# Optimization experiments

Measured on AMD Instinct MI355X. Metric: run time of the kernel, lower is better.

Reference implementation:

```python
import math
import jax, jax.numpy as jnp
from jax import lax
import numpy as np

B, T, DIM = 2, 1024, 512
EXPAND, D_STATE, CONV_K, NUM_SCALES = 2, 16, 4, 3
D_INNER = EXPAND * DIM
DT_RANK = D_INNER // 16


def parallel_scan_log(log_coeffs, log_values):
    # h_t = a_t*h_{t-1} + b_t via Heinsen log-space scan
    a_star = jnp.cumsum(log_coeffs, axis=1)
    return jnp.exp(a_star + lax.cumlogsumexp(log_values - a_star, axis=1))


def selective_scan(x, dt, A, B_ssm, C_ssm, D_p):
    Bb, Tt, di = x.shape
    ds = A.shape[1]
    dt = jax.nn.softplus(dt)
    dA = jnp.exp(dt[..., None] * A[None, None])                    # (B,T,di,ds)
    dBx = dt[..., None] * B_ssm[:, :, None, :] * x[..., None]      # (B,T,di,ds)
    log_dA = jnp.log(jnp.maximum(dA, 1e-38)).reshape(Bb, Tt, di * ds)
    log_dBx = jnp.log(jnp.maximum(dBx, 1e-38)).reshape(Bb, Tt, di * ds)
    h = parallel_scan_log(log_dA, log_dBx).reshape(Bb, Tt, di, ds)
    return jnp.einsum('bts,btds->btd', C_ssm, h) + D_p * x


def ssm_core(x, conv_w, conv_b, xproj_w, dtproj_w, dtproj_b, A_log, D_p):
    di = x.shape[-1]
    # depthwise causal conv1d: left-pad K-1 (== torch pad K-1 both sides + truncate to T)
    xc = lax.conv_general_dilated(x.transpose(0, 2, 1), conv_w, (1,), [(CONV_K - 1, 0)],
                                  dimension_numbers=('NCH', 'OIH', 'NCH'),
                                  feature_group_count=di)
    xc = jax.nn.silu((xc + conv_b[None, :, None]).transpose(0, 2, 1))
    proj = xc @ xproj_w.T
    dt_raw = proj[..., :DT_RANK]
    B_ssm = proj[..., DT_RANK:DT_RANK + D_STATE]
    C_ssm = proj[..., DT_RANK + D_STATE:]
    dt = dt_raw @ dtproj_w.T + dtproj_b
    A = -jnp.exp(A_log)
    return selective_scan(xc, dt, A, B_ssm, C_ssm, D_p)


def downsample(x, stride):
    if stride == 1:
        return x
    Bb, Tt, Dd = x.shape
    Tt2 = Tt // stride * stride
    return x[:, :Tt2].reshape(Bb, Tt2 // stride, stride, Dd).mean(axis=2)


def upsample(x, T_target):
    Bb, T_src, Dd = x.shape
    if T_src == T_target:
        return x
    factor = math.ceil(T_target / T_src)
    x_up = jnp.repeat(x, factor, axis=1)[:, :T_target]
    if x_up.shape[1] < T_target:
        pad = jnp.broadcast_to(x_up[:, -1:], (Bb, T_target - x_up.shape[1], Dd))
        x_up = jnp.concatenate([x_up, pad], axis=1)
    return x_up


def forward(x, in_proj_w, conv_w, conv_b, xproj_w, dtproj_w, dtproj_b, A_log, D_p,
            scale_weights, cg_w1, cg_w2, out_proj_w, ln_gamma, ln_beta):
    Tt = x.shape[1]
    residual = x
    xz = x @ in_proj_w.T
    x_in, gate = xz[..., :D_INNER], xz[..., D_INNER:]
    outs = []
    for s in range(NUM_SCALES):
        x_s = downsample(x_in, 2 ** s)
        y_s = ssm_core(x_s, conv_w[s], conv_b[s], xproj_w[s], dtproj_w[s],
                       dtproj_b[s], A_log[s], D_p[s])
        outs.append(upsample(y_s, Tt))
    w = jax.nn.softmax(scale_weights)
    fused = sum(w[s] * outs[s] for s in range(NUM_SCALES))
    ctx = jnp.mean(jnp.stack(outs, axis=0), axis=0)
    cg = jax.nn.sigmoid(jax.nn.silu(ctx @ cg_w1.T) @ cg_w2.T)
    fused = fused * cg
    out = (fused * jax.nn.silu(gate)) @ out_proj_w.T
    y = out + residual
    mu = jnp.mean(y, axis=-1, keepdims=True)
    var = jnp.var(y, axis=-1, keepdims=True)
    return (y - mu) / jnp.sqrt(var + 1e-5) * ln_gamma + ln_beta


def setup_inputs():
    key = jax.random.key(0)
    ks = jax.random.split(key, 12)
    x = jax.random.normal(ks[0], (B, T, DIM), jnp.float32)
    in_proj_w = jax.random.normal(ks[1], (2 * D_INNER, DIM), jnp.float32) * (1.0 / math.sqrt(DIM))
    conv_w = jax.random.normal(ks[2], (NUM_SCALES, D_INNER, 1, CONV_K), jnp.float32) * 0.3
    conv_b = jax.random.normal(ks[3], (NUM_SCALES, D_INNER), jnp.float32) * 0.05
    xproj_w = jax.random.normal(ks[4], (NUM_SCALES, DT_RANK + 2 * D_STATE, D_INNER), jnp.float32) * 0.02
    dtproj_w = jax.random.normal(ks[5], (NUM_SCALES, D_INNER, DT_RANK), jnp.float32) * 0.05
    dtproj_b = jax.random.uniform(ks[6], (NUM_SCALES, D_INNER), jnp.float32,
                                  math.log(0.001), math.log(0.1))
    A_log = jnp.broadcast_to(jnp.log(jnp.arange(1, D_STATE + 1, dtype=jnp.float32)),
                             (NUM_SCALES, D_INNER, D_STATE))
    D_p = jnp.ones((NUM_SCALES, D_INNER), jnp.float32)
    scale_weights = jnp.ones((NUM_SCALES,), jnp.float32)
    cg_w1 = jax.random.normal(ks[7], (D_INNER // 2, D_INNER), jnp.float32) * (1.0 / math.sqrt(D_INNER))
    cg_w2 = jax.random.normal(ks[8], (D_INNER, D_INNER // 2), jnp.float32) * (1.0 / math.sqrt(D_INNER // 2))
    out_proj_w = jax.random.normal(ks[9], (DIM, D_INNER), jnp.float32) * (1.0 / math.sqrt(D_INNER))
    ln_gamma = jnp.ones((DIM,), jnp.float32)
    ln_beta = jnp.zeros((DIM,), jnp.float32)
    return {"x": x, "in_proj_w": in_proj_w, "conv_w": conv_w, "conv_b": conv_b,
            "xproj_w": xproj_w, "dtproj_w": dtproj_w, "dtproj_b": dtproj_b,
            "A_log": A_log, "D_p": D_p, "scale_weights": scale_weights,
            "cg_w1": cg_w1, "cg_w2": cg_w2, "out_proj_w": out_proj_w,
            "ln_gamma": ln_gamma, "ln_beta": ln_beta}


def reference(x, in_proj_w, conv_w, conv_b, xproj_w, dtproj_w, dtproj_b, A_log, D_p,
              scale_weights, cg_w1, cg_w2, out_proj_w, ln_gamma, ln_beta):
    return forward(x, in_proj_w, conv_w, conv_b, xproj_w, dtproj_w, dtproj_b, A_log,
                   D_p, scale_weights, cg_w1, cg_w2, out_proj_w, ln_gamma, ln_beta)
```

## Files before the change

### kernel.cpp

```cpp
#include <hip/hip_runtime.h>
#include <hip/hip_bf16.h>

#define BATCH   2
#define SEQ     1024
#define DIMSZ   512
#define DINNER  1024
#define DTRANK  64
#define DSTATE  16
#define CHUNK   32

typedef __hip_bfloat16 bf16;
typedef __attribute__((ext_vector_type(8))) short s8v;
typedef __attribute__((ext_vector_type(4))) float f4v;

constexpr size_t OXI   = 0;
constexpr size_t OIPI  = 2097152;
constexpr size_t OXWI  = 4194304;
constexpr size_t ODTI  = 4784128;
constexpr size_t OC1I  = 5177344;
constexpr size_t OC2I  = 6225920;
constexpr size_t OOPI  = 7274496;
constexpr size_t OPJI  = 8323072;
constexpr size_t OH1I  = 8781824;
constexpr size_t OFGI  = 10878976;

__device__ __forceinline__ float sigmoidf_(float x) { return 1.f / (1.f + __expf(-x)); }
__device__ __forceinline__ float siluf_(float x) { return x * sigmoidf_(x); }
__device__ __forceinline__ void split2(float v, bf16& hi, bf16& lo) {
    hi = __float2bfloat16(v);
    lo = __float2bfloat16(v - __bfloat162float(hi));
}
__device__ __forceinline__ void split_store4i(const float4 v, bf16* __restrict__ p) {
    union { bf16 b[8]; uint4 q; } U;
    split2(v.x, U.b[0], U.b[4]); split2(v.y, U.b[1], U.b[5]);
    split2(v.z, U.b[2], U.b[6]); split2(v.w, U.b[3], U.b[7]);
    *reinterpret_cast<uint4*>(p) = U.q;
}
__device__ __forceinline__ void split_store4(const float4 v,
                                             bf16* __restrict__ ph,
                                             bf16* __restrict__ pl) {
    union { bf16 b[4]; uint2 u; } H, L;
    split2(v.x, H.b[0], L.b[0]); split2(v.y, H.b[1], L.b[1]);
    split2(v.z, H.b[2], L.b[2]); split2(v.w, H.b[3], L.b[3]);
    *reinterpret_cast<uint2*>(ph) = H.u;
    *reinterpret_cast<uint2*>(pl) = L.u;
}

__global__ void split_inputs_kernel(
    const float* __restrict__ x,   const float* __restrict__ ipw,
    const float* __restrict__ xw,  const float* __restrict__ dtw,
    const float* __restrict__ c1,  const float* __restrict__ c2,
    const float* __restrict__ opw, bf16* __restrict__ bws)
{
    int blk = blockIdx.x;
    const float* src; size_t off;
    if (blk < 1024)      { src = x;   off = OXI;  }
    else if (blk < 2048) { src = ipw; off = OIPI; blk -= 1024; }
    else if (blk < 2336) { src = xw;  off = OXWI; blk -= 2048; }
    else if (blk < 2528) { src = dtw; off = ODTI; blk -= 2336; }
    else if (blk < 3040) { src = c1;  off = OC1I; blk -= 2528; }
    else if (blk < 3552) { src = c2;  off = OC2I; blk -= 3040; }
    else                 { src = opw; off = OOPI; blk -= 3552; }
    int i = blk * 1024 + threadIdx.x * 4;
    float4 v = *reinterpret_cast<const float4*>(src + i);
    split_store4i(v, bws + off + (size_t)i * 2);
}

template <int ACT, bool ADD_RES, bool DT_MODE, bool CTX_A, bool GATE3, bool OUT_SPLIT>
__global__ __launch_bounds__(256) void mgemm_kernel(
    const bf16* __restrict__ Ai, int lda, int K,
    const bf16* __restrict__ Bi,
    const float* __restrict__ bias,
    const float* __restrict__ res,
    const float* __restrict__ gxz,
    const float* __restrict__ yy0,
    const float* __restrict__ yy1,
    const float* __restrict__ yy2,
    const float* __restrict__ swp,
    float* __restrict__ C, bf16* __restrict__ Ci, int N)
{
    __shared__ bf16 Ah[64][72], Al[64][72], Bh[64][72], Bl[64][72];

    const int m0 = blockIdx.x * 64;
    const int n0 = blockIdx.y * 64;
    const int tid = threadIdx.x;
    const int wave = tid >> 6;
    const int lane = tid & 63;
    const int wm = (wave >> 1) * 32;
    const int wn = (wave & 1) * 32;
    const int m16 = lane & 15;
    const int q   = lane >> 4;

    int scale = 0;
    if (DT_MODE) scale = (m0 < 2048) ? 0 : ((m0 < 3072) ? 1 : 2);
    const bf16* Bip = DT_MODE ? (Bi + (size_t)scale * 1024 * K * 2) : Bi;
    const float* bias_p = (ACT == 3) ? (DT_MODE ? bias + (size_t)scale * N : bias) : nullptr;

    f4v acc[2][2];
#pragma unroll
    for (int i = 0; i < 2; i++)
#pragma unroll
        for (int j = 0; j < 2; j++)
#pragma unroll
            for (int r = 0; r < 4; r++) acc[i][j][r] = 0.f;

    const int cch = tid & 15;
    const int c4  = cch * 4;
    const int r0  = tid >> 4;

    const float* a0p[4]; const float* a1p[4]; const float* a2p[4];
    const bf16*  aip[4];
#pragma unroll
    for (int p = 0; p < 4; p++) {
        int m = m0 + r0 + p * 16;
        if (CTX_A) {
            int b = m >> 10, t = m & 1023;
            a0p[p] = yy0 + (size_t)m * 1024 + c4;
            a1p[p] = yy1 + (size_t)((b << 9) + (t >> 1)) * 1024 + c4;
            a2p[p] = yy2 + (size_t)((b << 8) + (t >> 2)) * 1024 + c4;
        } else {
            aip[p] = Ai + ((size_t)m * lda + c4) * 2;
        }
    }
    const bf16* Bi_b = Bip + ((size_t)(n0 + r0) * K + c4) * 2;

    const int nkt = K >> 6;
    float4 raf[4]; uint2 rah[4], ral[4], rbh[4], rbl[4];
#pragma unroll
    for (int p = 0; p < 4; p++) {
        if (CTX_A) {
            float4 u = *reinterpret_cast<const float4*>(a0p[p]);
            float4 v = *reinterpret_cast<const float4*>(a1p[p]);
            float4 w = *reinterpret_cast<const float4*>(a2p[p]);
            raf[p] = make_float4((u.x + v.x + w.x) * (1.f / 3.f), (u.y + v.y + w.y) * (1.f / 3.f),
                                 (u.z + v.z + w.z) * (1.f / 3.f), (u.w + v.w + w.w) * (1.f / 3.f));
        } else {
            uint4 ua = *reinterpret_cast<const uint4*>(aip[p]);
            rah[p] = make_uint2(ua.x, ua.y); ral[p] = make_uint2(ua.z, ua.w);
        }
        uint4 ub = *reinterpret_cast<const uint4*>(Bi_b + (size_t)(p * 16) * K * 2);
        rbh[p] = make_uint2(ub.x, ub.y); rbl[p] = make_uint2(ub.z, ub.w);
    }

    for (int kt = 0; kt < nkt; kt++) {
        if (kt) __syncthreads();
#pragma unroll
        for (int p = 0; p < 4; p++) {
            int r = r0 + p * 16;
            if (CTX_A) {
                split_store4(raf[p], &Ah[r][c4], &Al[r][c4]);
            } else {
                *reinterpret_cast<uint2*>(&Ah[r][c4]) = rah[p];
                *reinterpret_cast<uint2*>(&Al[r][c4]) = ral[p];
            }
            *reinterpret_cast<uint2*>(&Bh[r][c4]) = rbh[p];
            *reinterpret_cast<uint2*>(&Bl[r][c4]) = rbl[p];
        }
        __syncthreads();
        if (kt + 1 < nkt) {
            int off = (kt + 1) * 64;
#pragma unroll
            for (int p = 0; p < 4; p++) {
                if (CTX_A) {
                    float4 u = *reinterpret_cast<const float4*>(a0p[p] + off);
                    float4 v = *reinterpret_cast<const float4*>(a1p[p] + off);
                    float4 w = *reinterpret_cast<const float4*>(a2p[p] + off);
                    raf[p] = make_float4((u.x + v.x + w.x) * (1.f / 3.f), (u.y + v.y + w.y) * (1.f / 3.f),
                                         (u.z + v.z + w.z) * (1.f / 3.f), (u.w + v.w + w.w) * (1.f / 3.f));
                } else {
                    uint4 ua = *reinterpret_cast<const uint4*>(aip[p] + (size_t)off * 2);
                    rah[p] = make_uint2(ua.x, ua.y); ral[p] = make_uint2(ua.z, ua.w);
                }
                uint4 ub = *reinterpret_cast<const uint4*>(Bi_b + ((size_t)(p * 16) * K + off) * 2);
                rbh[p] = make_uint2(ub.x, ub.y); rbl[p] = make_uint2(ub.z, ub.w);
            }
        }
#pragma unroll
        for (int kk = 0; kk < 2; kk++) {
            const int col = kk * 32 + q * 8;
            s8v ah[2], al[2], bh[2], bl[2];
#pragma unroll
            for (int i = 0; i < 2; i++) {
                int ar = wm + i * 16 + m16;
                ah[i] = *reinterpret_cast<const s8v*>(&Ah[ar][col]);
                al[i] = *reinterpret_cast<const s8v*>(&Al[ar][col]);
                int br = wn + i * 16 + m16;
                bh[i] = *reinterpret_cast<const s8v*>(&Bh[br][col]);
                bl[i] = *reinterpret_cast<const s8v*>(&Bl[br][col]);
            }
#pragma unroll
            for (int i = 0; i < 2; i++)
#pragma unroll
                for (int j = 0; j < 2; j++) {
                    acc[i][j] = __builtin_amdgcn_mfma_f32_16x16x32_bf16(ah[i], bh[j], acc[i][j], 0, 0, 0);
                    acc[i][j] = __builtin_amdgcn_mfma_f32_16x16x32_bf16(al[i], bh[j], acc[i][j], 0, 0, 0);
                    acc[i][j] = __builtin_amdgcn_mfma_f32_16x16x32_bf16(ah[i], bl[j], acc[i][j], 0, 0, 0);
                }
        }
    }

    float e0 = 0.f, e1 = 0.f, e2 = 0.f, inv = 0.f;
    if (GATE3) {
        float s0 = swp[0], s1 = swp[1], s2 = swp[2];
        float mx = fmaxf(s0, fmaxf(s1, s2));
        e0 = __expf(s0 - mx); e1 = __expf(s1 - mx); e2 = __expf(s2 - mx);
        inv = 1.f / (e0 + e1 + e2);
    }

#pragma unroll
    for (int i = 0; i < 2; i++) {
#pragma unroll
        for (int j = 0; j < 2; j++) {
#pragma unroll
            for (int r = 0; r < 4; r++) {
                int gm = m0 + wm + i * 16 + q * 4 + r;
                int gn = n0 + wn + j * 16 + m16;
                float v = acc[i][j][r];
                if (ACT == 3) { v += bias_p[gn]; v = (v > 20.f) ? v : __logf(1.f + __expf(v)); }
                else if (ACT == 1) v = siluf_(v);
                else if (ACT == 2) v = sigmoidf_(v);
                if (GATE3) {
                    int b = gm >> 10, t = gm & 1023;
                    float f = (e0 * yy0[(size_t)gm * 1024 + gn]
                             + e1 * yy1[(size_t)((b << 9) + (t >> 1)) * 1024 + gn]
                             + e2 * yy2[(size_t)((b << 8) + (t >> 2)) * 1024 + gn]) * inv;
                    v = f * v * siluf_(gxz[(size_t)gm * 2048 + 1024 + gn]);
                } else if (ADD_RES) {
                    v += res[(size_t)gm * N + gn];
                }
                if (OUT_SPLIT) {
                    bf16 hh, ll; split2(v, hh, ll);
                    size_t gb = ((size_t)gm * N + (gn & ~3)) * 2 + (gn & 3);
                    Ci[gb] = hh;
                    Ci[gb + 4] = ll;
                } else {
                    C[(size_t)gm * N + gn] = v;
                }
            }
        }
    }
}

__global__ __launch_bounds__(256) void xproj_mfma_kernel(
    const float* __restrict__ A,
    const bf16* __restrict__ xwi,
    float* __restrict__ pj, bf16* __restrict__ pjdti)
{
    const int K = 1024;
    __shared__ bf16 Ah[64][72], Al[64][72], Bh[64][72], Bl[64][72];

    const int m0 = blockIdx.x * 64;
    const int n0 = blockIdx.y * 64;
    const int tid = threadIdx.x;
    const int wave = tid >> 6;
    const int lane = tid & 63;
    const int wm = (wave >> 1) * 32;
    const int wn = (wave & 1) * 32;
    const int m16 = lane & 15;
    const int q   = lane >> 4;

    const int scale = (m0 < 2048) ? 0 : ((m0 < 3072) ? 1 : 2);
    const bf16* Bip = xwi + (size_t)scale * 96 * K * 2;

    f4v acc[2][2];
#pragma unroll
    for (int i = 0; i < 2; i++)
#pragma unroll
        for (int j = 0; j < 2; j++)
#pragma unroll
            for (int r = 0; r < 4; r++) acc[i][j][r] = 0.f;

    const int cch = tid & 15;
    const int c4  = cch * 4;
    const int r0  = tid >> 4;

    const float* Abase = A + (size_t)(m0 + r0) * K + c4;
    const bf16* Bi_b = Bip + ((size_t)(n0 + r0) * K + c4) * 2;
    bool bok[4];
#pragma unroll
    for (int p = 0; p < 4; p++) bok[p] = (n0 + r0 + p * 16) < 96;

    const int nkt = K >> 6;
    float4 ra[4]; uint2 rbh[4], rbl[4];
#pragma unroll
    for (int p = 0; p < 4; p++) {
        ra[p] = *reinterpret_cast<const float4*>(Abase + (size_t)(p * 16) * K);
        if (bok[p]) {
            uint4 ub = *reinterpret_cast<const uint4*>(Bi_b + (size_t)(p * 16) * K * 2);
            rbh[p] = make_uint2(ub.x, ub.y); rbl[p] = make_uint2(ub.z, ub.w);
        } else { rbh[p] = make_uint2(0u, 0u); rbl[p] = make_uint2(0u, 0u); }
    }

    for (int kt = 0; kt < nkt; kt++) {
        if (kt) __syncthreads();
#pragma unroll
        for (int p = 0; p < 4; p++) {
            int r = r0 + p * 16;
            split_store4(ra[p], &Ah[r][c4], &Al[r][c4]);
            *reinterpret_cast<uint2*>(&Bh[r][c4]) = rbh[p];
            *reinterpret_cast<uint2*>(&Bl[r][c4]) = rbl[p];
        }
        __syncthreads();
        if (kt + 1 < nkt) {
            int off = (kt + 1) * 64;
#pragma unroll
            for (int p = 0; p < 4; p++) {
                ra[p] = *reinterpret_cast<const float4*>(Abase + off + (size_t)(p * 16) * K);
                if (bok[p]) {
                    uint4 ub = *reinterpret_cast<const uint4*>(Bi_b + ((size_t)(p * 16) * K + off) * 2);
                    rbh[p] = make_uint2(ub.x, ub.y); rbl[p] = make_uint2(ub.z, ub.w);
                }
            }
        }
#pragma unroll
        for (int kk = 0; kk < 2; kk++) {
            const int col = kk * 32 + q * 8;
            s8v ah[2], al[2], bh[2], bl[2];
#pragma unroll
            for (int i = 0; i < 2; i++) {
                int ar = wm + i * 16 + m16;
                ah[i] = *reinterpret_cast<const s8v*>(&Ah[ar][col]);
                al[i] = *reinterpret_cast<const s8v*>(&Al[ar][col]);
                int br = wn + i * 16 + m16;
                bh[i] = *reinterpret_cast<const s8v*>(&Bh[br][col]);
                bl[i] = *reinterpret_cast<const s8v*>(&Bl[br][col]);
            }
#pragma unroll
            for (int i = 0; i < 2; i++)
#pragma unroll
                for (int j = 0; j < 2; j++) {
                    acc[i][j] = __builtin_amdgcn_mfma_f32_16x16x32_bf16(ah[i], bh[j], acc[i][j], 0, 0, 0);
                    acc[i][j] = __builtin_amdgcn_mfma_f32_16x16x32_bf16(al[i], bh[j], acc[i][j], 0, 0, 0);
                    acc[i][j] = __builtin_amdgcn_mfma_f32_16x16x32_bf16(ah[i], bl[j], acc[i][j], 0, 0, 0);
                }
        }
    }

#pragma unroll
    for (int i = 0; i < 2; i++) {
#pragma unroll
        for (int j = 0; j < 2; j++) {
            int gn = n0 + wn + j * 16 + m16;
            if (gn >= 96) continue;
#pragma unroll
            for (int r = 0; r < 4; r++) {
                int gm = m0 + wm + i * 16 + q * 4 + r;
                float v = acc[i][j][r];
                pj[(size_t)gm * 96 + gn] = v;
                if (gn < 64) {
                    bf16 hh, ll; split2(v, hh, ll);
                    size_t gb = ((size_t)gm * 64 + (gn & ~3)) * 2 + (gn & 3);
                    pjdti[gb] = hh;
                    pjdti[gb + 4] = ll;
                }
            }
        }
    }
}

__global__ void conv_fused_kernel(const float* __restrict__ xz,
                                  const float* __restrict__ cw,
                                  const float* __restrict__ cb,
                                  float* __restrict__ xc)
{
    int idx = blockIdx.x * blockDim.x + threadIdx.x;
    if (idx >= 3670016) return;
    int s, rel;
    if (idx < 2097152)      { s = 0; rel = idx; }
    else if (idx < 3145728) { s = 1; rel = idx - 2097152; }
    else                    { s = 2; rel = idx - 3145728; }
    int c = rel & 1023;
    int row = rel >> 10;
    int Ts = 1024 >> s;
    int b = row / Ts;
    int t = row - b * Ts;
    const float* base = xz + (size_t)(b * 1024) * 2048 + c;

    float acc = cb[s * 1024 + c];
#pragma unroll
    for (int k = 0; k < 4; k++) {
        int tau = t - 3 + k;
        if (tau < 0) continue;
        float xv;
        if (s == 0) {
            xv = base[(size_t)tau * 2048];
        } else if (s == 1) {
            xv = 0.5f * (base[(size_t)(2 * tau) * 2048] + base[(size_t)(2 * tau + 1) * 2048]);
        } else {
            xv = 0.25f * (base[(size_t)(4 * tau) * 2048] + base[(size_t)(4 * tau + 1) * 2048]
                        + base[(size_t)(4 * tau + 2) * 2048] + base[(size_t)(4 * tau + 3) * 2048]);
        }
        acc = fmaf(cw[(s * 1024 + c) * 4 + k], xv, acc);
    }
    xc[idx] = siluf_(acc);
}

__device__ __forceinline__ void scan_decode(int blk, int& s, int& nchunk, int& Ts,
                                            int& dquad, int& chunk, int& b, size_t& soff)
{
    int local;
    if (blk < 256)      { s = 0; local = blk;       soff = 0; }
    else if (blk < 384) { s = 1; local = blk - 256; soff = 1048576; }
    else                { s = 2; local = blk - 384; soff = 1572864; }
    nchunk = 32 >> s;
    Ts = 1024 >> s;
    dquad = local & 3;
    chunk = (local >> 2) & (nchunk - 1);
    b = local >> (7 - s);
}

__global__ __launch_bounds__(256) void scan_pass1(
    const float* __restrict__ dt0, const float* __restrict__ xc0, const float* __restrict__ pj0,
    const float* __restrict__ dt1, const float* __restrict__ xc1, const float* __restrict__ pj1,
    const float* __restrict__ dt2, const float* __restrict__ xc2, const float* __restrict__ pj2,
    const float* __restrict__ A_log,
    float* __restrict__ prodA_buf, float* __restrict__ h_buf)
{
    const int jhalf = (blockIdx.x >= 448) ? 1 : 0;
    const int jo = jhalf * 8;
    int s, nchunk, Ts, dquad, chunk, b; size_t soff;
    scan_decode(blockIdx.x - jhalf * 448, s, nchunk, Ts, dquad, chunk, b, soff);
    const float* dt = (s == 0) ? dt0 : (s == 1) ? dt1 : dt2;
    const float* xc = (s == 0) ? xc0 : (s == 1) ? xc1 : xc2;
    const float* pj = (s == 0) ? pj0 : (s == 1) ? pj1 : pj2;

    const int d = dquad * 256 + threadIdx.x;
    const size_t rowbase = (size_t)b * Ts;
    const int t0 = chunk * CHUNK;

    float Acoef[8], h[8], p[8];
#pragma unroll
    for (int j = 0; j < 8; j++) {
        Acoef[j] = -__expf(A_log[((size_t)(s * DINNER + d)) * 16 + jo + j]);
        h[j] = 0.f; p[j] = 1.f;
    }

    __shared__ float bcB[CHUNK][8];
    if (threadIdx.x < CHUNK * 8) {
        int i = threadIdx.x >> 3, jj = threadIdx.x & 7;
        bcB[i][jj] = pj[(rowbase + t0 + i) * 96 + 64 + jo + jj];
    }
    __syncthreads();

    for (int i = 0; i < CHUNK; i++) {
        size_t t = rowbase + t0 + i;
        float dtv = dt[t * DINNER + d];
        float xv  = xc[t * DINNER + d];
#pragma unroll
        for (int j = 0; j < 8; j++) {
            float dA  = fmaxf(__expf(dtv * Acoef[j]), 1e-38f);
            float dbx = fmaxf(dtv * bcB[i][j] * xv, 1e-38f);
            h[j] = fmaf(dA, h[j], dbx);
            p[j] *= dA;
        }
    }

    size_t base = soff + (size_t)((b * nchunk + chunk) * 16 + jo) * 1024 + d;
#pragma unroll
    for (int j = 0; j < 8; j++) {
        prodA_buf[base + (size_t)j * 1024] = p[j];
        h_buf[base + (size_t)j * 1024] = h[j];
    }
}

__global__ __launch_bounds__(256) void scan_prefix_kernel(
    const float* __restrict__ prodA_buf, float* __restrict__ h_buf)
{
    int blk = blockIdx.x;
    int s; size_t soff;
    if (blk < 128)      { s = 0; soff = 0; }
    else if (blk < 256) { s = 1; soff = 1048576; blk -= 128; }
    else                { s = 2; soff = 1572864; blk -= 256; }
    const int nchunk = 32 >> s;
    const int b  = blk >> 6;
    const int j  = (blk >> 2) & 15;
    const int dq = blk & 3;
    const int d  = dq * 256 + threadIdx.x;

    float H = 0.f;
    for (int c = 0; c < nchunk; c++) {
        size_t idx = soff + (size_t)((b * nchunk + c) * 16 + j) * 1024 + d;
        float p = prodA_buf[idx];
        float h = h_buf[idx];
        h_buf[idx] = H;
        H = fmaf(p, H, h);
    }
}

__global__ __launch_bounds__(256) void scan_pass2(
    const float* __restrict__ dt0, const float* __restrict__ xc0,
    const float* __restrict__ pj0,
    const float* __restrict__ dt1, const float* __restrict__ xc1,
    const float* __restrict__ pj1,
    const float* __restrict__ dt2, const float* __restrict__ xc2,
    const float* __restrict__ pj2,
    float* __restrict__ y0, float* __restrict__ y1, float* __restrict__ y2,
    const float* __restrict__ A_log, const float* __restrict__ D_p,
    const float* __restrict__ carry)
{
    int s, nchunk, Ts, dquad, chunk, b; size_t soff;
    scan_decode(blockIdx.x, s, nchunk, Ts, dquad, chunk, b, soff);
    const float* dt = (s == 0) ? dt0 : (s == 1) ? dt1 : dt2;
    const float* xc = (s == 0) ? xc0 : (s == 1) ? xc1 : xc2;
    const float* pj = (s == 0) ? pj0 : (s == 1) ? pj1 : pj2;
    float* y = (s == 0) ? y0 : (s == 1) ? y1 : y2;

    const int d = dquad * 256 + threadIdx.x;
    const size_t rowbase = (size_t)b * Ts;
    const int t0 = chunk * CHUNK;

    float Acoef[16], h[16];
    const size_t cb = soff + (size_t)((b * nchunk + chunk) * 16) * 1024 + d;
#pragma unroll
    for (int j = 0; j < 16; j++) {
        Acoef[j] = -__expf(A_log[((size_t)(s * DINNER + d)) * 16 + j]);
        h[j] = carry[cb + (size_t)j * 1024];
    }
    const float Dp = D_p[s * DINNER + d];

    __shared__ float bc[CHUNK][32];
    for (int u = threadIdx.x; u < CHUNK * 32; u += 256) {
        int i = u >> 5, jj = u & 31;
        bc[i][jj] = pj[(rowbase + t0 + i) * 96 + 64 + jj];
    }
    __syncthreads();

    for (int i = 0; i < CHUNK; i++) {
        size_t t = rowbase + t0 + i;
        float dtv = dt[t * DINNER + d];
        float xv  = xc[t * DINNER + d];
        float accy = 0.f;
#pragma unroll
        for (int j = 0; j < 16; j++) {
            float dA  = fmaxf(__expf(dtv * Acoef[j]), 1e-38f);
            float dbx = fmaxf(dtv * bc[i][j] * xv, 1e-38f);
            h[j] = fmaf(dA, h[j], dbx);
            accy = fmaf(bc[i][16 + j], h[j], accy);
        }
        y[t * DINNER + d] = accy + Dp * xv;
    }
}

__global__ __launch_bounds__(256) void ln_kernel(
    const float* __restrict__ yin, const float* __restrict__ gamma,
    const float* __restrict__ beta, float* __restrict__ out)
{
    int token = blockIdx.x;
    int tid = threadIdx.x;
    const float* row = yin + (size_t)token * DIMSZ;
    float v0 = row[tid], v1 = row[tid + 256];
    __shared__ float s1[256], s2[256];
    s1[tid] = v0 + v1;
    s2[tid] = v0 * v0 + v1 * v1;
    __syncthreads();
    for (int off = 128; off > 0; off >>= 1) {
        if (tid < off) { s1[tid] += s1[tid + off]; s2[tid] += s2[tid + off]; }
        __syncthreads();
    }
    float mu = s1[0] * (1.f / 512.f);
    float var = s2[0] * (1.f / 512.f) - mu * mu;
    float rstd = rsqrtf(var + 1e-5f);
    float* orow = out + (size_t)token * DIMSZ;
    orow[tid]       = (v0 - mu) * rstd * gamma[tid]       + beta[tid];
    orow[tid + 256] = (v1 - mu) * rstd * gamma[tid + 256] + beta[tid + 256];
}

extern "C" void kernel_launch(void* const* d_in, const int* in_sizes, int n_in,
                              void* d_out, int out_size, void* d_ws, size_t ws_size,
                              hipStream_t stream)
{
    const float* x         = (const float*)d_in[0];
    const float* in_proj_w = (const float*)d_in[1];
    const float* conv_w    = (const float*)d_in[2];
    const float* conv_b    = (const float*)d_in[3];
    const float* xproj_w   = (const float*)d_in[4];
    const float* dtproj_w  = (const float*)d_in[5];
    const float* dtproj_b  = (const float*)d_in[6];
    const float* A_log     = (const float*)d_in[7];
    const float* D_p       = (const float*)d_in[8];
    const float* scale_w   = (const float*)d_in[9];
    const float* cg_w1     = (const float*)d_in[10];
    const float* cg_w2     = (const float*)d_in[11];
    const float* out_pw    = (const float*)d_in[12];
    const float* ln_gamma  = (const float*)d_in[13];
    const float* ln_beta   = (const float*)d_in[14];
    float* out = (float*)d_out;

    float* ws = (float*)d_ws;
    float* xz    = ws;
    float* xc0   = xz    + 4194304;
    float* xc1   = xc0   + 2097152;
    float* xc2   = xc1   + 1048576;
    float* pj0   = xc2   + 524288;
    float* pj1   = pj0   + 196608;
    float* pj2   = pj1   + 98304;
    float* dt0   = pj2   + 49152;
    float* dt1   = dt0   + 2097152;
    float* dt2   = dt1   + 1048576;
    float* y0    = dt2   + 524288;
    float* y1    = y0    + 2097152;
    float* y2    = y1    + 1048576;
    float* prodA = y2    + 524288 + 3670016;
    float* hbuf  = prodA + 1835008;

    bf16* bws = (bf16*)(ws + 23887872);
    const bf16 *xi   = bws + OXI;
    const bf16 *ipwi = bws + OIPI;
    const bf16 *xwi  = bws + OXWI;
    const bf16 *dtwi = bws + ODTI;
    const bf16 *c1i  = bws + OC1I;
    const bf16 *c2i  = bws + OC2I;
    const bf16 *opwi = bws + OOPI;
    bf16 *pjdti = bws + OPJI;
    bf16 *h1i   = bws + OH1I;
    bf16 *fgi   = bws + OFGI;

    float* outpre = prodA;

    split_inputs_kernel<<<4064, 256, 0, stream>>>(
        x, in_proj_w, xproj_w, dtproj_w, cg_w1, cg_w2, out_pw, bws);

    mgemm_kernel<0, false, false, false, false, false><<<dim3(32, 32), 256, 0, stream>>>(
        xi, DIMSZ, DIMSZ, ipwi, nullptr, nullptr, nullptr,
        nullptr, nullptr, nullptr, nullptr, xz, nullptr, 2048);

    conv_fused_kernel<<<14336, 256, 0, stream>>>(xz, conv_w, conv_b, xc0);

    xproj_mfma_kernel<<<dim3(56, 2), 256, 0, stream>>>(xc0, xwi, pj0, pjdti);

    mgemm_kernel<3, false, true, false, false, false><<<dim3(56, 16), 256, 0, stream>>>(
        pjdti, DTRANK, DTRANK, dtwi, dtproj_b, nullptr, nullptr,
        nullptr, nullptr, nullptr, nullptr, dt0, nullptr, 1024);

    scan_pass1<<<896, 256, 0, stream>>>(dt0, xc0, pj0, dt1, xc1, pj1,
                                        dt2, xc2, pj2, A_log, prodA, hbuf);
    scan_prefix_kernel<<<384, 256, 0, stream>>>(prodA, hbuf);
    scan_pass2<<<448, 256, 0, stream>>>(dt0, xc0, pj0, dt1, xc1, pj1,
                                        dt2, xc2, pj2,
                                        y0, y1, y2, A_log, D_p, hbuf);

    mgemm_kernel<1, false, false, true, false, true><<<dim3(32, 8), 256, 0, stream>>>(
        nullptr, DINNER, DINNER, c1i, nullptr, nullptr, nullptr,
        y0, y1, y2, nullptr, nullptr, h1i, 512);

    mgemm_kernel<2, false, false, false, true, true><<<dim3(32, 16), 256, 0, stream>>>(
        h1i, DIMSZ, DIMSZ, c2i, nullptr, nullptr, xz,
        y0, y1, y2, scale_w, nullptr, fgi, 1024);

    mgemm_kernel<0, true, false, false, false, false><<<dim3(32, 8), 256, 0, stream>>>(
        fgi, DINNER, DINNER, opwi, nullptr, x, nullptr,
        nullptr, nullptr, nullptr, nullptr, outpre, nullptr, 512);

    ln_kernel<<<BATCH * SEQ, 256, 0, stream>>>(outpre, ln_gamma, ln_beta, out);
}
```

Measured before the change: 284.5 us.

## Enlarge GEMM tiles to 128x128 with a workgroup swizzle

Replaces the 64x64 split-bf16 MFMA GEMM with a 128x128 tile. Each wave now computes a 64x64 sub-tile using a 4x4 accumulator grid, and each K step covers 32 instead of 64. Block IDs are remapped by an 8-way swizzle to spread neighbouring tiles, and all five GEMM launches get correspondingly smaller grids. The aim is more operand reuse per LDS load and less global traffic per output. The cost is far fewer workgroups (as few as 64 for the N=512 GEMMs), which can leave much of the GPU idle, plus higher register pressure.

```diff
diff --git a/kernel.cpp b/kernel.cpp
--- a/kernel.cpp
+++ b/kernel.cpp
@@ -67,7 +67,7 @@
 }
 
 template <int ACT, bool ADD_RES, bool DT_MODE, bool CTX_A, bool GATE3, bool OUT_SPLIT>
-__global__ __launch_bounds__(256) void mgemm_kernel(
+__global__ __launch_bounds__(256) void mgemm2_kernel(
     const bf16* __restrict__ Ai, int lda, int K,
     const bf16* __restrict__ Bi,
     const float* __restrict__ bias,
@@ -79,15 +79,20 @@
     const float* __restrict__ swp,
     float* __restrict__ C, bf16* __restrict__ Ci, int N)
 {
-    __shared__ bf16 Ah[64][72], Al[64][72], Bh[64][72], Bl[64][72];
-
-    const int m0 = blockIdx.x * 64;
-    const int n0 = blockIdx.y * 64;
+    __shared__ bf16 Ah[128][40], Al[128][40], Bh[128][40], Bl[128][40];
+
+    const int gx = gridDim.x;
+    const int nwg = gx * gridDim.y;
+    int bid = blockIdx.y * gx + blockIdx.x;
+    bid = (bid & 7) * (nwg >> 3) + (bid >> 3);
+    const int m0 = (bid % gx) * 128;
+    const int n0 = (bid / gx) * 128;
+
     const int tid = threadIdx.x;
     const int wave = tid >> 6;
     const int lane = tid & 63;
-    const int wm = (wave >> 1) * 32;
-    const int wn = (wave & 1) * 32;
+    const int wm = (wave >> 1) * 64;
+    const int wn = (wave & 1) * 64;
     const int m16 = lane & 15;
     const int q   = lane >> 4;
 
@@ -96,106 +101,93 @@
     const bf16* Bip = DT_MODE ? (Bi + (size_t)scale * 1024 * K * 2) : Bi;
     const float* bias_p = (ACT == 3) ? (DT_MODE ? bias + (size_t)scale * N : bias) : nullptr;
 
-    f4v acc[2][2];
-#pragma unroll
-    for (int i = 0; i < 2; i++)
-#pragma unroll
-        for (int j = 0; j < 2; j++)
+    f4v acc[4][4];
+#pragma unroll
+    for (int i = 0; i < 4; i++)
+#pragma unroll
+        for (int j = 0; j < 4; j++)
 #pragma unroll
             for (int r = 0; r < 4; r++) acc[i][j][r] = 0.f;
 
-    const int cch = tid & 15;
-    const int c4  = cch * 4;
-    const int r0  = tid >> 4;
-
-    const float* a0p[4]; const float* a1p[4]; const float* a2p[4];
-    const bf16*  aip[4];
-#pragma unroll
-    for (int p = 0; p < 4; p++) {
-        int m = m0 + r0 + p * 16;
-        if (CTX_A) {
-            int b = m >> 10, t = m & 1023;
-            a0p[p] = yy0 + (size_t)m * 1024 + c4;
-            a1p[p] = yy1 + (size_t)((b << 9) + (t >> 1)) * 1024 + c4;
-            a2p[p] = yy2 + (size_t)((b << 8) + (t >> 2)) * 1024 + c4;
-        } else {
-            aip[p] = Ai + ((size_t)m * lda + c4) * 2;
-        }
-    }
-    const bf16* Bi_b = Bip + ((size_t)(n0 + r0) * K + c4) * 2;
-
-    const int nkt = K >> 6;
-    float4 raf[4]; uint2 rah[4], ral[4], rbh[4], rbl[4];
+    const int sr = tid >> 1;
+    const int kh = (tid & 1) * 16;
+
+    const bf16* Aip = CTX_A ? nullptr : (Ai + ((size_t)(m0 + sr) * lda + kh) * 2);
+    const bf16* Bib = Bip + ((size_t)(n0 + sr) * K + kh) * 2;
+    const float *a0p = nullptr, *a1p = nullptr, *a2p = nullptr;
+    if (CTX_A) {
+        int m = m0 + sr;
+        int b = m >> 10, t = m & 1023;
+        a0p = yy0 + (size_t)m * 1024 + kh;
+        a1p = yy1 + (size_t)((b << 9) + (t >> 1)) * 1024 + kh;
+        a2p = yy2 + (size_t)((b << 8) + (t >> 2)) * 1024 + kh;
+    }
+
+    const int nkt = K >> 5;
+    float4 raf[4]; uint4 ra[4], rb[4];
 #pragma unroll
     for (int p = 0; p < 4; p++) {
         if (CTX_A) {
-            float4 u = *reinterpret_cast<const float4*>(a0p[p]);
-            float4 v = *reinterpret_cast<const float4*>(a1p[p]);
-            float4 w = *reinterpret_cast<const float4*>(a2p[p]);
+            float4 u = *reinterpret_cast<const float4*>(a0p + p * 4);
+            float4 v = *reinterpret_cast<const float4*>(a1p + p * 4);
+            float4 w = *reinterpret_cast<const float4*>(a2p + p * 4);
             raf[p] = make_float4((u.x + v.x + w.x) * (1.f / 3.f), (u.y + v.y + w.y) * (1.f / 3.f),
                                  (u.z + v.z + w.z) * (1.f / 3.f), (u.w + v.w + w.w) * (1.f / 3.f));
         } else {
-            uint4 ua = *reinterpret_cast<const uint4*>(aip[p]);
-            rah[p] = make_uint2(ua.x, ua.y); ral[p] = make_uint2(ua.z, ua.w);
-        }
-        uint4 ub = *reinterpret_cast<const uint4*>(Bi_b + (size_t)(p * 16) * K * 2);
-        rbh[p] = make_uint2(ub.x, ub.y); rbl[p] = make_uint2(ub.z, ub.w);
+            ra[p] = *reinterpret_cast<const uint4*>(Aip + (size_t)p * 8);
+        }
+        rb[p] = *reinterpret_cast<const uint4*>(Bib + (size_t)p * 8);
     }
 
     for (int kt = 0; kt < nkt; kt++) {
         if (kt) __syncthreads();
 #pragma unroll
         for (int p = 0; p < 4; p++) {
-            int r = r0 + p * 16;
+            int c = kh + p * 4;
             if (CTX_A) {
-                split_store4(raf[p], &Ah[r][c4], &Al[r][c4]);
+                split_store4(raf[p], &Ah[sr][c], &Al[sr][c]);
             } else {
-                *reinterpret_cast<uint2*>(&Ah[r][c4]) = rah[p];
-                *reinterpret_cast<uint2*>(&Al[r][c4]) = ral[p];
+                *reinterpret_cast<uint2*>(&Ah[sr][c]) = make_uint2(ra[p].x, ra[p].y);
+                *reinterpret_cast<uint2*>(&Al[sr][c]) = make_uint2(ra[p].z, ra[p].w);
             }
-            *reinterpret_cast<uint2*>(&Bh[r][c4]) = rbh[p];
-            *reinterpret_cast<uint2*>(&Bl[r][c4]) = rbl[p];
+            *reinterpret_cast<uint2*>(&Bh[sr][c]) = make_uint2(rb[p].x, rb[p].y);
+            *reinterpret_cast<uint2*>(&Bl[sr][c]) = make_uint2(rb[p].z, rb[p].w);
         }
         __syncthreads();
         if (kt + 1 < nkt) {
-            int off = (kt + 1) * 64;
+            int off = (kt + 1) * 32;
 #pragma unroll
             for (int p = 0; p < 4; p++) {
                 if (CTX_A) {
-                    float4 u = *reinterpret_cast<const float4*>(a0p[p] + off);
-                    float4 v = *reinterpret_cast<const float4*>(a1p[p] + off);
-                    float4 w = *reinterpret_cast<const float4*>(a2p[p] + off);
+                    float4 u = *reinterpret_cast<const float4*>(a0p + off + p * 4);
+                    float4 v = *reinterpret_cast<const float4*>(a1p + off + p * 4);
+                    float4 w = *reinterpret_cast<const float4*>(a2p + off + p * 4);
                     raf[p] = make_float4((u.x + v.x + w.x) * (1.f / 3.f), (u.y + v.y + w.y) * (1.f / 3.f),
                                          (u.z + v.z + w.z) * (1.f / 3.f), (u.w + v.w + w.w) * (1.f / 3.f));
                 } else {
-                    uint4 ua = *reinterpret_cast<const uint4*>(aip[p] + (size_t)off * 2);
-                    rah[p] = make_uint2(ua.x, ua.y); ral[p] = make_uint2(ua.z, ua.w);
+                    ra[p] = *reinterpret_cast<const uint4*>(Aip + (size_t)off * 2 + p * 8);
                 }
-                uint4 ub = *reinterpret_cast<const uint4*>(Bi_b + ((size_t)(p * 16) * K + off) * 2);
-                rbh[p] = make_uint2(ub.x, ub.y); rbl[p] = make_uint2(ub.z, ub.w);
+                rb[p] = *reinterpret_cast<const uint4*>(Bib + (size_t)off * 2 + p * 8);
             }
         }
-#pragma unroll
-        for (int kk = 0; kk < 2; kk++) {
-            const int col = kk * 32 + q * 8;
-            s8v ah[2], al[2], bh[2], bl[2];
-#pragma unroll
-            for (int i = 0; i < 2; i++) {
-                int ar = wm + i * 16 + m16;
-                ah[i] = *reinterpret_cast<const s8v*>(&Ah[ar][col]);
-                al[i] = *reinterpret_cast<const s8v*>(&Al[ar][col]);
-                int br = wn + i * 16 + m16;
-                bh[i] = *reinterpret_cast<const s8v*>(&Bh[br][col]);
-                bl[i] = *reinterpret_cast<const s8v*>(&Bl[br][col]);
+        s8v ah[4], al[4];
+#pragma unroll
+        for (int i = 0; i < 4; i++) {
+            int ar = wm + i * 16 + m16;
+            ah[i] = *reinterpret_cast<const s8v*>(&Ah[ar][q * 8]);
+            al[i] = *reinterpret_cast<const s8v*>(&Al[ar][q * 8]);
+        }
+#pragma unroll
+        for (int j = 0; j < 4; j++) {
+            int br = wn + j * 16 + m16;
+            s8v bh = *reinterpret_cast<const s8v*>(&Bh[br][q * 8]);
+            s8v bl = *reinterpret_cast<const s8v*>(&Bl[br][q * 8]);
+#pragma unroll
+            for (int i = 0; i < 4; i++) {
+                acc[i][j] = __builtin_amdgcn_mfma_f32_16x16x32_bf16(ah[i], bh, acc[i][j], 0, 0, 0);
+                acc[i][j] = __builtin_amdgcn_mfma_f32_16x16x32_bf16(al[i], bh, acc[i][j], 0, 0, 0);
+                acc[i][j] = __builtin_amdgcn_mfma_f32_16x16x32_bf16(ah[i], bl, acc[i][j], 0, 0, 0);
             }
-#pragma unroll
-            for (int i = 0; i < 2; i++)
-#pragma unroll
-                for (int j = 0; j < 2; j++) {
-                    acc[i][j] = __builtin_amdgcn_mfma_f32_16x16x32_bf16(ah[i], bh[j], acc[i][j], 0, 0, 0);
-                    acc[i][j] = __builtin_amdgcn_mfma_f32_16x16x32_bf16(al[i], bh[j], acc[i][j], 0, 0, 0);
-                    acc[i][j] = __builtin_amdgcn_mfma_f32_16x16x32_bf16(ah[i], bl[j], acc[i][j], 0, 0, 0);
-                }
         }
     }
 
@@ -208,9 +200,9 @@
     }
 
 #pragma unroll
-    for (int i = 0; i < 2; i++) {
-#pragma unroll
-        for (int j = 0; j < 2; j++) {
+    for (int i = 0; i < 4; i++) {
+#pragma unroll
+        for (int j = 0; j < 4; j++) {
 #pragma unroll
             for (int r = 0; r < 4; r++) {
                 int gm = m0 + wm + i * 16 + q * 4 + r;
@@ -620,7 +612,7 @@
     split_inputs_kernel<<<4064, 256, 0, stream>>>(
         x, in_proj_w, xproj_w, dtproj_w, cg_w1, cg_w2, out_pw, bws);
 
-    mgemm_kernel<0, false, false, false, false, false><<<dim3(32, 32), 256, 0, stream>>>(
+    mgemm2_kernel<0, false, false, false, false, false><<<dim3(16, 16), 256, 0, stream>>>(
         xi, DIMSZ, DIMSZ, ipwi, nullptr, nullptr, nullptr,
         nullptr, nullptr, nullptr, nullptr, xz, nullptr, 2048);
 
@@ -628,7 +620,7 @@
 
     xproj_mfma_kernel<<<dim3(56, 2), 256, 0, stream>>>(xc0, xwi, pj0, pjdti);
 
-    mgemm_kernel<3, false, true, false, false, false><<<dim3(56, 16), 256, 0, stream>>>(
+    mgemm2_kernel<3, false, true, false, false, false><<<dim3(28, 8), 256, 0, stream>>>(
         pjdti, DTRANK, DTRANK, dtwi, dtproj_b, nullptr, nullptr,
         nullptr, nullptr, nullptr, nullptr, dt0, nullptr, 1024);
 
@@ -639,15 +631,15 @@
                                         dt2, xc2, pj2,
                                         y0, y1, y2, A_log, D_p, hbuf);
 
-    mgemm_kernel<1, false, false, true, false, true><<<dim3(32, 8), 256, 0, stream>>>(
+    mgemm2_kernel<1, false, false, true, false, true><<<dim3(16, 4), 256, 0, stream>>>(
         nullptr, DINNER, DINNER, c1i, nullptr, nullptr, nullptr,
         y0, y1, y2, nullptr, nullptr, h1i, 512);
 
-    mgemm_kernel<2, false, false, false, true, true><<<dim3(32, 16), 256, 0, stream>>>(
+    mgemm2_kernel<2, false, false, false, true, true><<<dim3(16, 8), 256, 0, stream>>>(
         h1i, DIMSZ, DIMSZ, c2i, nullptr, nullptr, xz,
         y0, y1, y2, scale_w, nullptr, fgi, 1024);
 
-    mgemm_kernel<0, true, false, false, false, false><<<dim3(32, 8), 256, 0, stream>>>(
+    mgemm2_kernel<0, true, false, false, false, false><<<dim3(16, 4), 256, 0, stream>>>(
         fgi, DINNER, DINNER, opwi, nullptr, x, nullptr,
         nullptr, nullptr, nullptr, nullptr, outpre, nullptr, 512);
 
```

New measurement: 380.0 us. 33.5% more time.

## Split-K the low-occupancy GEMMs and fuse partial reductions into consumers

Applied to the files above, without the earlier changes.

The x-projection, first context-gate GEMM and output projection now run split-K with two K halves on blockIdx.z, each writing a partial fp32 result. The partials are summed by a new combine kernel for the projection, by the next GEMM's A-loader (which now applies SiLU after adding both halves), and by the LayerNorm kernel. The aim is to double the block count for GEMMs whose grids (112 or 256 blocks) underfill the GPU. The cost is extra partial-buffer traffic and one added launch.

```diff
diff --git a/kernel.cpp b/kernel.cpp
--- a/kernel.cpp
+++ b/kernel.cpp
@@ -21,7 +21,6 @@
 constexpr size_t OC2I  = 6225920;
 constexpr size_t OOPI  = 7274496;
 constexpr size_t OPJI  = 8323072;
-constexpr size_t OH1I  = 8781824;
 constexpr size_t OFGI  = 10878976;
 
 __device__ __forceinline__ float sigmoidf_(float x) { return 1.f / (1.f + __expf(-x)); }
@@ -66,9 +65,9 @@
     split_store4i(v, bws + off + (size_t)i * 2);
 }
 
-template <int ACT, bool ADD_RES, bool DT_MODE, bool CTX_A, bool GATE3, bool OUT_SPLIT>
+template <int ACT, bool ADD_RES, bool DT_MODE, int AMODE, bool GATE3, bool OUT_SPLIT>
 __global__ __launch_bounds__(256) void mgemm_kernel(
-    const bf16* __restrict__ Ai, int lda, int K,
+    const bf16* __restrict__ Ai, int lda, int K, int ldb,
     const bf16* __restrict__ Bi,
     const float* __restrict__ bias,
     const float* __restrict__ res,
@@ -76,6 +75,8 @@
     const float* __restrict__ yy0,
     const float* __restrict__ yy1,
     const float* __restrict__ yy2,
+    const float* __restrict__ sa0,
+    const float* __restrict__ sa1,
     const float* __restrict__ swp,
     float* __restrict__ C, bf16* __restrict__ Ci, int N)
 {
@@ -83,6 +84,9 @@
 
     const int m0 = blockIdx.x * 64;
     const int n0 = blockIdx.y * 64;
+    const int kz = blockIdx.z;
+    const int koff = kz * K;
+    const size_t coff = (size_t)kz * (size_t)(gridDim.x * 64) * N;
     const int tid = threadIdx.x;
     const int wave = tid >> 6;
     const int lane = tid & 63;
@@ -93,7 +97,7 @@
 
     int scale = 0;
     if (DT_MODE) scale = (m0 < 2048) ? 0 : ((m0 < 3072) ? 1 : 2);
-    const bf16* Bip = DT_MODE ? (Bi + (size_t)scale * 1024 * K * 2) : Bi;
+    const bf16* Bip = DT_MODE ? (Bi + (size_t)scale * 1024 * ldb * 2) : Bi;
     const float* bias_p = (ACT == 3) ? (DT_MODE ? bias + (size_t)scale * N : bias) : nullptr;
 
     f4v acc[2][2];
@@ -109,36 +113,45 @@
     const int r0  = tid >> 4;
 
     const float* a0p[4]; const float* a1p[4]; const float* a2p[4];
+    const float* s0p[4]; const float* s1p[4];
     const bf16*  aip[4];
 #pragma unroll
     for (int p = 0; p < 4; p++) {
         int m = m0 + r0 + p * 16;
-        if (CTX_A) {
+        if (AMODE == 1) {
             int b = m >> 10, t = m & 1023;
-            a0p[p] = yy0 + (size_t)m * 1024 + c4;
-            a1p[p] = yy1 + (size_t)((b << 9) + (t >> 1)) * 1024 + c4;
-            a2p[p] = yy2 + (size_t)((b << 8) + (t >> 2)) * 1024 + c4;
+            a0p[p] = yy0 + koff + (size_t)m * 1024 + c4;
+            a1p[p] = yy1 + koff + (size_t)((b << 9) + (t >> 1)) * 1024 + c4;
+            a2p[p] = yy2 + koff + (size_t)((b << 8) + (t >> 2)) * 1024 + c4;
+        } else if (AMODE == 2) {
+            s0p[p] = sa0 + koff + (size_t)m * lda + c4;
+            s1p[p] = sa1 + koff + (size_t)m * lda + c4;
         } else {
-            aip[p] = Ai + ((size_t)m * lda + c4) * 2;
-        }
-    }
-    const bf16* Bi_b = Bip + ((size_t)(n0 + r0) * K + c4) * 2;
+            aip[p] = Ai + ((size_t)m * lda + koff + c4) * 2;
+        }
+    }
+    const bf16* Bi_b = Bip + ((size_t)(n0 + r0) * ldb + koff + c4) * 2;
 
     const int nkt = K >> 6;
     float4 raf[4]; uint2 rah[4], ral[4], rbh[4], rbl[4];
 #pragma unroll
     for (int p = 0; p < 4; p++) {
-        if (CTX_A) {
+        if (AMODE == 1) {
             float4 u = *reinterpret_cast<const float4*>(a0p[p]);
             float4 v = *reinterpret_cast<const float4*>(a1p[p]);
             float4 w = *reinterpret_cast<const float4*>(a2p[p]);
             raf[p] = make_float4((u.x + v.x + w.x) * (1.f / 3.f), (u.y + v.y + w.y) * (1.f / 3.f),
                                  (u.z + v.z + w.z) * (1.f / 3.f), (u.w + v.w + w.w) * (1.f / 3.f));
+        } else if (AMODE == 2) {
+            float4 u = *reinterpret_cast<const float4*>(s0p[p]);
+            float4 v = *reinterpret_cast<const float4*>(s1p[p]);
+            raf[p] = make_float4(siluf_(u.x + v.x), siluf_(u.y + v.y),
+                                 siluf_(u.z + v.z), siluf_(u.w + v.w));
         } else {
             uint4 ua = *reinterpret_cast<const uint4*>(aip[p]);
             rah[p] = make_uint2(ua.x, ua.y); ral[p] = make_uint2(ua.z, ua.w);
         }
-        uint4 ub = *reinterpret_cast<const uint4*>(Bi_b + (size_t)(p * 16) * K * 2);
+        uint4 ub = *reinterpret_cast<const uint4*>(Bi_b + (size_t)(p * 16) * ldb * 2);
         rbh[p] = make_uint2(ub.x, ub.y); rbl[p] = make_uint2(ub.z, ub.w);
     }
 
@@ -147,7 +160,7 @@
 #pragma unroll
         for (int p = 0; p < 4; p++) {
             int r = r0 + p * 16;
-            if (CTX_A) {
+            if (AMODE != 0) {
                 split_store4(raf[p], &Ah[r][c4], &Al[r][c4]);
             } else {
                 *reinterpret_cast<uint2*>(&Ah[r][c4]) = rah[p];
@@ -161,17 +174,22 @@
             int off = (kt + 1) * 64;
 #pragma unroll
             for (int p = 0; p < 4; p++) {
-                if (CTX_A) {
+                if (AMODE == 1) {
                     float4 u = *reinterpret_cast<const float4*>(a0p[p] + off);
                     float4 v = *reinterpret_cast<const float4*>(a1p[p] + off);
                     float4 w = *reinterpret_cast<const float4*>(a2p[p] + off);
                     raf[p] = make_float4((u.x + v.x + w.x) * (1.f / 3.f), (u.y + v.y + w.y) * (1.f / 3.f),
                                          (u.z + v.z + w.z) * (1.f / 3.f), (u.w + v.w + w.w) * (1.f / 3.f));
+                } else if (AMODE == 2) {
+                    float4 u = *reinterpret_cast<const float4*>(s0p[p] + off);
+                    float4 v = *reinterpret_cast<const float4*>(s1p[p] + off);
+                    raf[p] = make_float4(siluf_(u.x + v.x), siluf_(u.y + v.y),
+                                         siluf_(u.z + v.z), siluf_(u.w + v.w));
                 } else {
                     uint4 ua = *reinterpret_cast<const uint4*>(aip[p] + (size_t)off * 2);
                     rah[p] = make_uint2(ua.x, ua.y); ral[p] = make_uint2(ua.z, ua.w);
                 }
-                uint4 ub = *reinterpret_cast<const uint4*>(Bi_b + ((size_t)(p * 16) * K + off) * 2);
+                uint4 ub = *reinterpret_cast<const uint4*>(Bi_b + ((size_t)(p * 16) * ldb + off) * 2);
                 rbh[p] = make_uint2(ub.x, ub.y); rbl[p] = make_uint2(ub.z, ub.w);
             }
         }
@@ -226,7 +244,7 @@
                              + e2 * yy2[(size_t)((b << 8) + (t >> 2)) * 1024 + gn]) * inv;
                     v = f * v * siluf_(gxz[(size_t)gm * 2048 + 1024 + gn]);
                 } else if (ADD_RES) {
-                    v += res[(size_t)gm * N + gn];
+                    if (kz == 0) v += res[(size_t)gm * N + gn];
                 }
                 if (OUT_SPLIT) {
                     bf16 hh, ll; split2(v, hh, ll);
@@ -234,7 +252,7 @@
                     Ci[gb] = hh;
                     Ci[gb + 4] = ll;
                 } else {
-                    C[(size_t)gm * N + gn] = v;
+                    C[coff + (size_t)gm * N + gn] = v;
                 }
             }
         }
@@ -244,13 +262,14 @@
 __global__ __launch_bounds__(256) void xproj_mfma_kernel(
     const float* __restrict__ A,
     const bf16* __restrict__ xwi,
-    float* __restrict__ pj, bf16* __restrict__ pjdti)
-{
-    const int K = 1024;
+    float* __restrict__ pjp)
+{
     __shared__ bf16 Ah[64][72], Al[64][72], Bh[64][72], Bl[64][72];
 
     const int m0 = blockIdx.x * 64;
     const int n0 = blockIdx.y * 64;
+    const int kz = blockIdx.z;
+    const int koff = kz * 512;
     const int tid = threadIdx.x;
     const int wave = tid >> 6;
     const int lane = tid & 63;
@@ -260,7 +279,7 @@
     const int q   = lane >> 4;
 
     const int scale = (m0 < 2048) ? 0 : ((m0 < 3072) ? 1 : 2);
-    const bf16* Bip = xwi + (size_t)scale * 96 * K * 2;
+    const bf16* Bip = xwi + (size_t)scale * 96 * 1024 * 2;
 
     f4v acc[2][2];
 #pragma unroll
@@ -274,19 +293,19 @@
     const int c4  = cch * 4;
     const int r0  = tid >> 4;
 
-    const float* Abase = A + (size_t)(m0 + r0) * K + c4;
-    const bf16* Bi_b = Bip + ((size_t)(n0 + r0) * K + c4) * 2;
+    const float* Abase = A + (size_t)(m0 + r0) * 1024 + koff + c4;
+    const bf16* Bi_b = Bip + ((size_t)(n0 + r0) * 1024 + koff + c4) * 2;
     bool bok[4];
 #pragma unroll
     for (int p = 0; p < 4; p++) bok[p] = (n0 + r0 + p * 16) < 96;
 
-    const int nkt = K >> 6;
+    const int nkt = 8;
     float4 ra[4]; uint2 rbh[4], rbl[4];
 #pragma unroll
     for (int p = 0; p < 4; p++) {
-        ra[p] = *reinterpret_cast<const float4*>(Abase + (size_t)(p * 16) * K);
+        ra[p] = *reinterpret_cast<const float4*>(Abase + (size_t)(p * 16) * 1024);
         if (bok[p]) {
-            uint4 ub = *reinterpret_cast<const uint4*>(Bi_b + (size_t)(p * 16) * K * 2);
+            uint4 ub = *reinterpret_cast<const uint4*>(Bi_b + (size_t)(p * 16) * 1024 * 2);
             rbh[p] = make_uint2(ub.x, ub.y); rbl[p] = make_uint2(ub.z, ub.w);
         } else { rbh[p] = make_uint2(0u, 0u); rbl[p] = make_uint2(0u, 0u); }
     }
@@ -305,9 +324,9 @@
             int off = (kt + 1) * 64;
 #pragma unroll
             for (int p = 0; p < 4; p++) {
-                ra[p] = *reinterpret_cast<const float4*>(Abase + off + (size_t)(p * 16) * K);
+                ra[p] = *reinterpret_cast<const float4*>(Abase + off + (size_t)(p * 16) * 1024);
                 if (bok[p]) {
-                    uint4 ub = *reinterpret_cast<const uint4*>(Bi_b + ((size_t)(p * 16) * K + off) * 2);
+                    uint4 ub = *reinterpret_cast<const uint4*>(Bi_b + ((size_t)(p * 16) * 1024 + off) * 2);
                     rbh[p] = make_uint2(ub.x, ub.y); rbl[p] = make_uint2(ub.z, ub.w);
                 }
             }
@@ -336,6 +355,7 @@
         }
     }
 
+    float* out = pjp + (size_t)kz * 344064;
 #pragma unroll
     for (int i = 0; i < 2; i++) {
 #pragma unroll
@@ -345,17 +365,26 @@
 #pragma unroll
             for (int r = 0; r < 4; r++) {
                 int gm = m0 + wm + i * 16 + q * 4 + r;
-                float v = acc[i][j][r];
-                pj[(size_t)gm * 96 + gn] = v;
-                if (gn < 64) {
-                    bf16 hh, ll; split2(v, hh, ll);
-                    size_t gb = ((size_t)gm * 64 + (gn & ~3)) * 2 + (gn & 3);
-                    pjdti[gb] = hh;
-                    pjdti[gb + 4] = ll;
-                }
+                out[(size_t)gm * 96 + gn] = acc[i][j][r];
             }
         }
     }
+}
+
+__global__ void combine_pj_kernel(const float* __restrict__ pjp,
+                                  float* __restrict__ pj,
+                                  bf16* __restrict__ pjdti)
+{
+    int g = blockIdx.x * 256 + threadIdx.x;
+    if (g >= 86016) return;
+    int gm = g / 24;
+    int gc = (g % 24) * 4;
+    size_t o = (size_t)gm * 96 + gc;
+    float4 a = *reinterpret_cast<const float4*>(pjp + o);
+    float4 b = *reinterpret_cast<const float4*>(pjp + 344064 + o);
+    float4 s = make_float4(a.x + b.x, a.y + b.y, a.z + b.z, a.w + b.w);
+    *reinterpret_cast<float4*>(pj + o) = s;
+    if (gc < 64) split_store4i(s, pjdti + ((size_t)gm * 64 + gc) * 2);
 }
 
 __global__ void conv_fused_kernel(const float* __restrict__ xz,
@@ -542,13 +571,15 @@
 }
 
 __global__ __launch_bounds__(256) void ln_kernel(
-    const float* __restrict__ yin, const float* __restrict__ gamma,
+    const float* __restrict__ ya, const float* __restrict__ yb,
+    const float* __restrict__ gamma,
     const float* __restrict__ beta, float* __restrict__ out)
 {
     int token = blockIdx.x;
     int tid = threadIdx.x;
-    const float* row = yin + (size_t)token * DIMSZ;
-    float v0 = row[tid], v1 = row[tid + 256];
+    size_t o = (size_t)token * DIMSZ;
+    float v0 = ya[o + tid] + yb[o + tid];
+    float v1 = ya[o + tid + 256] + yb[o + tid + 256];
     __shared__ float s1[256], s2[256];
     s1[tid] = v0 + v1;
     s2[tid] = v0 * v0 + v1 * v1;
@@ -560,7 +591,7 @@
     float mu = s1[0] * (1.f / 512.f);
     float var = s2[0] * (1.f / 512.f) - mu * mu;
     float rstd = rsqrtf(var + 1e-5f);
-    float* orow = out + (size_t)token * DIMSZ;
+    float* orow = out + o;
     orow[tid]       = (v0 - mu) * rstd * gamma[tid]       + beta[tid];
     orow[tid + 256] = (v1 - mu) * rstd * gamma[tid + 256] + beta[tid + 256];
 }
@@ -600,8 +631,13 @@
     float* y0    = dt2   + 524288;
     float* y1    = y0    + 2097152;
     float* y2    = y1    + 1048576;
-    float* prodA = y2    + 524288 + 3670016;
+    float* hole  = y2    + 524288;
+    float* prodA = hole  + 3670016;
     float* hbuf  = prodA + 1835008;
+
+    float* pjp   = hole;
+    float* h1p   = hole + 688128;
+    float* outp  = prodA;
 
     bf16* bws = (bf16*)(ws + 23887872);
     const bf16 *xi   = bws + OXI;
@@ -612,25 +648,24 @@
     const bf16 *c2i  = bws + OC2I;
     const bf16 *opwi = bws + OOPI;
     bf16 *pjdti = bws + OPJI;
-    bf16 *h1i   = bws + OH1I;
     bf16 *fgi   = bws + OFGI;
-
-    float* outpre = prodA;
 
     split_inputs_kernel<<<4064, 256, 0, stream>>>(
         x, in_proj_w, xproj_w, dtproj_w, cg_w1, cg_w2, out_pw, bws);
 
-    mgemm_kernel<0, false, false, false, false, false><<<dim3(32, 32), 256, 0, stream>>>(
-        xi, DIMSZ, DIMSZ, ipwi, nullptr, nullptr, nullptr,
-        nullptr, nullptr, nullptr, nullptr, xz, nullptr, 2048);
+    mgemm_kernel<0, false, false, 0, false, false><<<dim3(32, 32), 256, 0, stream>>>(
+        xi, 512, 512, 512, ipwi, nullptr, nullptr, nullptr,
+        nullptr, nullptr, nullptr, nullptr, nullptr, nullptr, xz, nullptr, 2048);
 
     conv_fused_kernel<<<14336, 256, 0, stream>>>(xz, conv_w, conv_b, xc0);
 
-    xproj_mfma_kernel<<<dim3(56, 2), 256, 0, stream>>>(xc0, xwi, pj0, pjdti);
-
-    mgemm_kernel<3, false, true, false, false, false><<<dim3(56, 16), 256, 0, stream>>>(
-        pjdti, DTRANK, DTRANK, dtwi, dtproj_b, nullptr, nullptr,
-        nullptr, nullptr, nullptr, nullptr, dt0, nullptr, 1024);
+    xproj_mfma_kernel<<<dim3(56, 2, 2), 256, 0, stream>>>(xc0, xwi, pjp);
+
+    combine_pj_kernel<<<336, 256, 0, stream>>>(pjp, pj0, pjdti);
+
+    mgemm_kernel<3, false, true, 0, false, false><<<dim3(56, 16), 256, 0, stream>>>(
+        pjdti, 64, 64, 64, dtwi, dtproj_b, nullptr, nullptr,
+        nullptr, nullptr, nullptr, nullptr, nullptr, nullptr, dt0, nullptr, 1024);
 
     scan_pass1<<<896, 256, 0, stream>>>(dt0, xc0, pj0, dt1, xc1, pj1,
                                         dt2, xc2, pj2, A_log, prodA, hbuf);
@@ -639,17 +674,18 @@
                                         dt2, xc2, pj2,
                                         y0, y1, y2, A_log, D_p, hbuf);
 
-    mgemm_kernel<1, false, false, true, false, true><<<dim3(32, 8), 256, 0, stream>>>(
-        nullptr, DINNER, DINNER, c1i, nullptr, nullptr, nullptr,
-        y0, y1, y2, nullptr, nullptr, h1i, 512);
-
-    mgemm_kernel<2, false, false, false, true, true><<<dim3(32, 16), 256, 0, stream>>>(
-        h1i, DIMSZ, DIMSZ, c2i, nullptr, nullptr, xz,
-        y0, y1, y2, scale_w, nullptr, fgi, 1024);
-
-    mgemm_kernel<0, true, false, false, false, false><<<dim3(32, 8), 256, 0, stream>>>(
-        fgi, DINNER, DINNER, opwi, nullptr, x, nullptr,
-        nullptr, nullptr, nullptr, nullptr, outpre, nullptr, 512);
-
-    ln_kernel<<<BATCH * SEQ, 256, 0, stream>>>(outpre, ln_gamma, ln_beta, out);
-}
+    mgemm_kernel<0, false, false, 1, false, false><<<dim3(32, 8, 2), 256, 0, stream>>>(
+        nullptr, 1024, 512, 1024, c1i, nullptr, nullptr, nullptr,
+        y0, y1, y2, nullptr, nullptr, nullptr, h1p, nullptr, 512);
+
+    mgemm_kernel<2, false, false, 2, true, true><<<dim3(32, 16), 256, 0, stream>>>(
+        nullptr, 512, 512, 512, c2i, nullptr, nullptr, xz,
+        y0, y1, y2, h1p, h1p + 1048576, scale_w, nullptr, fgi, 1024);
+
+    mgemm_kernel<0, true, false, 0, false, false><<<dim3(32, 8, 2), 256, 0, stream>>>(
+        fgi, 1024, 512, 1024, opwi, nullptr, x, nullptr,
+        nullptr, nullptr, nullptr, nullptr, nullptr, nullptr, outp, nullptr, 512);
+
+    ln_kernel<<<BATCH * SEQ, 256, 0, stream>>>(outp, outp + 1048576,
+                                               ln_gamma, ln_beta, out);
+}
```

After: 270.0 us. -5.1%, faster.
